# Kernel tuning notes

Measured on AMD Instinct MI355X. Metric: run time of the kernel, lower is better.

The kernel has to match this reference:

```python
import jax, jax.numpy as jnp
import numpy as np

B, T, F = 16, 1024, 512       # batch, time, input_dim
G, V, D = 2, 320, 128         # num_groups, num_vars, var_dim (quantized_dim // G)
TAU = 2.0                     # max_temp * decay**0 at num_updates=0
EPS = 1e-7


def setup_inputs() -> dict:
    key = jax.random.key(0)
    kx, kw, kc, kg = jax.random.split(key, 4)
    x = jax.random.normal(kx, (B, T, F), dtype=jnp.float32)
    w_proj = jax.random.normal(kw, (G * V, F), dtype=jnp.float32)  # NormalLinear: std=1
    b_proj = jnp.zeros((G * V,), dtype=jnp.float32)
    codebook = jax.random.uniform(kc, (1, G * V, D), dtype=jnp.float32)  # uniform init
    u = jax.random.uniform(kg, (B * T, G, V), dtype=jnp.float32, minval=1e-10, maxval=1.0)
    gumbel = -jnp.log(-jnp.log(u))
    return {"x": x, "w_proj": w_proj, "b_proj": b_proj, "codebook": codebook, "gumbel": gumbel}


def reference(x, w_proj, b_proj, codebook, gumbel):
    bsz, tsz, _ = x.shape
    # projection -> (B, T, G, V)
    logits = (jnp.einsum("btf,nf->btn", x, w_proj) + b_proj).reshape(bsz, tsz, G, V)

    # hard one-hot of argmax (float32), like scatter_
    k = jnp.argmax(logits, axis=-1)
    hard_x = jax.nn.one_hot(k, V, dtype=jnp.float32)  # (B, T, G, V)

    # code perplexity: mean over batch dim only, sum over (T, G)
    hard_probs = hard_x.mean(axis=0)  # (T, G, V)
    code_perplexity = jnp.exp(-jnp.sum(hard_probs * jnp.log(hard_probs + EPS), axis=-1)).sum()

    # prob perplexity: softmax over codes, mean over all tokens, sum over groups
    flat_logits = logits.reshape(bsz * tsz, G, V)
    avg_probs = jax.nn.softmax(flat_logits, axis=-1).mean(axis=0)  # (G, V)
    prob_perplexity = jnp.exp(-jnp.sum(avg_probs * jnp.log(avg_probs + EPS), axis=-1)).sum()

    # gumbel-softmax, hard=True with straight-through estimator (training path)
    y_soft = jax.nn.softmax((flat_logits + gumbel) / TAU, axis=-1)  # (N, G, V)
    idx = jnp.argmax(y_soft, axis=-1)
    y_hard = jax.nn.one_hot(idx, V, dtype=y_soft.dtype)
    y = y_hard + y_soft - jax.lax.stop_gradient(y_soft)  # (N, G, V)

    # broadcast-multiply + sum over codes == grouped gather/matmul against codebook
    cb_gvd = codebook.reshape(G, V, D)
    quantized = jnp.einsum("ngv,gvd->ngd", y, cb_gvd).reshape(bsz, tsz, G * D)
    return quantized, code_perplexity, prob_perplexity
```

## Files before the change

kernel.cpp:

```cpp
#include <hip/hip_runtime.h>
#include <math.h>

#define B_   16
#define T_   1024
#define F_   512
#define G_   2
#define V_   320
#define D_   128
#define N_   (B_ * T_)
#define GV   (G_ * V_)
#define EPS_ 1e-7f

#define ROWS    64
#define THREADS 512
#define NBLK    (N_ / ROWS)
#define NC      32

#define BOFF  0
#define AOFF  40960
#define BUFSZ 45056
#define LDSZ  (2 * BUFSZ)

typedef _Float16 half8 __attribute__((ext_vector_type(8)));
typedef _Float16 half2_t __attribute__((ext_vector_type(2)));
typedef float f32x16 __attribute__((ext_vector_type(16)));

#define GLDS16(g, l)                                                           \
  __builtin_amdgcn_global_load_lds(                                            \
      (const __attribute__((address_space(1))) unsigned int*)(g),              \
      (__attribute__((address_space(3))) unsigned int*)(l), 16, 0, 0)

#define CNTW      (T_ * G_ * (V_ / 2))
#define WS_COUNTS 0
#define WS_AVG    CNTW
#define WS_ENT    (WS_AVG + NBLK * GV)
#define WS_WPK    (WS_ENT + T_ * G_)
#define WS_AVGRED (WS_WPK + (GV * F_ * 2 / 2))

__global__ __launch_bounds__(640) void k_conv_w(
    const float* __restrict__ w, _Float16* __restrict__ wpk)
{
  const int cl = blockIdx.x;
  const int c = cl >> 1, limb = cl & 1;
#pragma unroll
  for (int it = 0; it < 2; ++it) {
    const int t2 = threadIdx.x + it * 640;
    const int n = t2 >> 6, ln = t2 & 63;
    const int row = n * 32 + (ln & 31);
    const int k0 = c * 16 + (ln >> 5) * 8;
    const float4 v0 = *(const float4*)(w + (size_t)row * F_ + k0);
    const float4 v1 = *(const float4*)(w + (size_t)row * F_ + k0 + 4);
    half8 h;
#pragma unroll
    for (int k = 0; k < 8; ++k) {
      const float vk = (k < 4) ? ((const float*)&v0)[k] : ((const float*)&v1)[k - 4];
      const _Float16 hk = (_Float16)vk;
      h[k] = limb ? (_Float16)((vk - (float)hk) * 2048.0f) : hk;
    }
    ((half8*)wpk)[((size_t)cl * 20 + n) * 64 + ln] = h;
  }
}

__global__ __launch_bounds__(THREADS, 2) void k_fused(
    const float* __restrict__ x, const _Float16* __restrict__ wpk,
    const float* __restrict__ bias, const float* __restrict__ cb,
    const float* __restrict__ gum, float* __restrict__ out,
    unsigned* __restrict__ counts, float* __restrict__ avg_part)
{
  __shared__ __align__(16) unsigned char SB[LDSZ];
  const int tid = threadIdx.x;
  const int wv  = tid >> 6;
  const int ln  = tid & 63;
  const int lo  = ln & 31, hi = ln >> 5;
  const int wvm = wv >> 2, wvn = wv & 3;
  const int blk = blockIdx.x;
  const int n0  = blk * ROWS;

  f32x16 ah_acc[5], al_acc[5];
#pragma unroll
  for (int t = 0; t < 5; ++t)
#pragma unroll
    for (int i = 0; i < 16; ++i) { ah_acc[t][i] = 0.0f; al_acc[t][i] = 0.0f; }

  const int arow = tid >> 3;
  const int akp  = tid & 7;
  const int awoff = (arow >> 5) * 1024 + (((akp >> 2) << 5) + (arow & 31)) * 16
                  + (akp & 3) * 4;
  const float2* x2 = (const float2*)x;
  const size_t xrowbase = (size_t)(n0 + arow) * (F_ / 2) + akp;

  const int aro_h = AOFF + 0 * 2048 + wvm * 1024 + ln * 16;
  const int aro_l = AOFF + 1 * 2048 + wvm * 1024 + ln * 16;
  int bro_h[5], bro_l[5];
#pragma unroll
  for (int t = 0; t < 5; ++t) {
    bro_h[t] = BOFF + (0 * 20 + wvn * 5 + t) * 1024 + ln * 16;
    bro_l[t] = BOFF + (1 * 20 + wvn * 5 + t) * 1024 + ln * 16;
  }

  {
    const float2 xv = x2[xrowbase + 0 * 8];
#pragma unroll
    for (int i = 0; i < 5; ++i) {
      const int seg = wv * 5 + i;
      GLDS16(wpk + ((size_t)(0 * 40 + seg) * 64 + ln) * 8, SB + BOFF + seg * 1024);
    }
    half2_t hh, hl;
#pragma unroll
    for (int k = 0; k < 2; ++k) {
      const float f = k ? xv.y : xv.x;
      const _Float16 h = (_Float16)f;
      hh[k] = h; hl[k] = (_Float16)((f - (float)h) * 2048.0f);
    }
    *(half2_t*)(SB + AOFF + awoff) = hh;
    *(half2_t*)(SB + AOFF + 2048 + awoff) = hl;
  }
  __builtin_amdgcn_sched_barrier(0);
  asm volatile("s_waitcnt vmcnt(0) lgkmcnt(0)" ::: "memory");
  __builtin_amdgcn_s_barrier();
  __builtin_amdgcn_sched_barrier(0);

  for (int cc = 0; cc < NC; ++cc) {
    unsigned char* curb = SB + (cc & 1) * BUFSZ;
    unsigned char* nxtb = SB + ((cc & 1) ^ 1) * BUFSZ;
    if (cc + 1 < NC) {
      const int c1 = cc + 1;
      const float2 xv = x2[xrowbase + c1 * 8];
#pragma unroll
      for (int i = 0; i < 5; ++i) {
        const int seg = wv * 5 + i;
        GLDS16(wpk + ((size_t)(c1 * 40 + seg) * 64 + ln) * 8,
               nxtb + BOFF + seg * 1024);
      }
      half2_t hh, hl;
#pragma unroll
      for (int k = 0; k < 2; ++k) {
        const float f = k ? xv.y : xv.x;
        const _Float16 h = (_Float16)f;
        hh[k] = h; hl[k] = (_Float16)((f - (float)h) * 2048.0f);
      }
      *(half2_t*)(nxtb + AOFF + awoff) = hh;
      *(half2_t*)(nxtb + AOFF + 2048 + awoff) = hl;
    }
    const half8 ah = *(const half8*)(curb + aro_h);
    const half8 al = *(const half8*)(curb + aro_l);
#pragma unroll
    for (int t = 0; t < 5; ++t) {
      const half8 bh = *(const half8*)(curb + bro_h[t]);
      const half8 bl = *(const half8*)(curb + bro_l[t]);
      ah_acc[t] = __builtin_amdgcn_mfma_f32_32x32x16_f16(ah, bh, ah_acc[t], 0, 0, 0);
      al_acc[t] = __builtin_amdgcn_mfma_f32_32x32x16_f16(al, bh, al_acc[t], 0, 0, 0);
      al_acc[t] = __builtin_amdgcn_mfma_f32_32x32x16_f16(ah, bl, al_acc[t], 0, 0, 0);
    }
    __builtin_amdgcn_sched_barrier(0);
    asm volatile("s_waitcnt vmcnt(0) lgkmcnt(0)" ::: "memory");
    __builtin_amdgcn_s_barrier();
    __builtin_amdgcn_sched_barrier(0);
  }

  float bfrag[5];
#pragma unroll
  for (int t = 0; t < 5; ++t) bfrag[t] = bias[wvn * 160 + t * 32 + lo];

  float racc[G_][5];
#pragma unroll
  for (int g = 0; g < G_; ++g)
#pragma unroll
    for (int j = 0; j < 5; ++j) racc[g][j] = 0.f;

  float* LBUF = (float*)SB;

#pragma unroll
  for (int R = 0; R < 4; ++R) {
    if (wvm == (R >> 1)) {
#pragma unroll
      for (int t = 0; t < 5; ++t) {
        const int col = wvn * 160 + t * 32 + lo;
#pragma unroll
        for (int rr = 0; rr < 8; ++rr) {
          const int reg  = ((R & 1) << 3) + rr;
          const int lrow = (rr & 3) + ((rr >> 2) << 3) + (hi << 2);
          LBUF[lrow * GV + col] =
              ah_acc[t][reg] + al_acc[t][reg] * (1.0f / 2048.0f) + bfrag[t];
        }
      }
    }
    __syncthreads();
#pragma unroll
    for (int rr2 = 0; rr2 < 2; ++rr2) {
      const int lrow = wv * 2 + rr2;
      const int n = n0 + R * 16 + lrow;
#pragma unroll
      for (int g = 0; g < G_; ++g) {
        float L[5], GU[5];
#pragma unroll
        for (int j = 0; j < 5; ++j) {
          L[j]  = LBUF[lrow * GV + g * V_ + 64 * j + ln];
          GU[j] = gum[(size_t)n * GV + g * V_ + 64 * j + ln];
        }
        float m1 = L[0];         int a1 = ln;
        float m2 = L[0] + GU[0]; int a2 = ln;
#pragma unroll
        for (int j = 1; j < 5; ++j) {
          const int cix = 64 * j + ln;
          if (L[j] > m1) { m1 = L[j]; a1 = cix; }
          const float t2 = L[j] + GU[j];
          if (t2 > m2) { m2 = t2; a2 = cix; }
        }
        for (int off = 32; off; off >>= 1) {
          float om = __shfl_down(m1, off); int oa = __shfl_down(a1, off);
          if (om > m1 || (om == m1 && oa < a1)) { m1 = om; a1 = oa; }
          float om2 = __shfl_down(m2, off); int oa2 = __shfl_down(a2, off);
          if (om2 > m2 || (om2 == m2 && oa2 < a2)) { m2 = om2; a2 = oa2; }
        }
        m1 = __shfl(m1, 0); a1 = __shfl(a1, 0); a2 = __shfl(a2, 0);

        float e[5], s = 0.f;
#pragma unroll
        for (int j = 0; j < 5; ++j) { e[j] = expf(L[j] - m1); s += e[j]; }
        for (int off = 32; off; off >>= 1) s += __shfl_down(s, off);
        s = __shfl(s, 0);
        const float inv = 1.0f / s;
#pragma unroll
        for (int j = 0; j < 5; ++j) racc[g][j] += e[j] * inv;

        if (ln == 0) {
          const int t = n & (T_ - 1);
          atomicAdd(&counts[(t * G_ + g) * (V_ / 2) + (a1 >> 1)],
                    1u << ((a1 & 1) * 16));
        }
        const float2* cbr = (const float2*)(cb + (size_t)(g * V_ + a2) * D_);
        float2* op = (float2*)(out + (size_t)n * (G_ * D_) + g * D_);
        op[ln] = cbr[ln];
      }
    }
    __syncthreads();
  }

  float* la = (float*)SB;
#pragma unroll
  for (int g = 0; g < G_; ++g)
#pragma unroll
    for (int j = 0; j < 5; ++j)
      la[wv * GV + g * V_ + 64 * j + ln] = racc[g][j];
  __syncthreads();
  for (int cix = tid; cix < GV; cix += THREADS) {
    float s = 0.f;
#pragma unroll
    for (int v = 0; v < 8; ++v) s += la[v * GV + cix];
    avg_part[(size_t)blk * GV + cix] = s;
  }
}

__global__ __launch_bounds__(256) void k_post(
    const unsigned* __restrict__ counts, float* __restrict__ ent,
    const float* __restrict__ avg_part, float* __restrict__ avgred)
{
  const int b = blockIdx.x;
  const int lane = threadIdx.x & 63;
  if (b < (T_ * G_) / 4) {
    const int item = b * 4 + (threadIdx.x >> 6);
    const unsigned* c = counts + (size_t)item * (V_ / 2);
    float s = 0.f;
#pragma unroll
    for (int j = 0; j < 3; ++j) {
      const int wi = lane + 64 * j;
      if (wi < V_ / 2) {
        const unsigned wd = c[wi];
        const float h0 = (float)(wd & 0xffffu) * (1.0f / B_);
        const float h1 = (float)(wd >> 16) * (1.0f / B_);
        s += h0 * logf(h0 + EPS_) + h1 * logf(h1 + EPS_);
      }
    }
    for (int off = 32; off; off >>= 1) s += __shfl_down(s, off);
    if (lane == 0) ent[item] = expf(-s);
  } else {
    const int cix = (b - (T_ * G_) / 4) * 4 + (threadIdx.x >> 6);
    float s = 0.f;
    for (int bb = lane; bb < NBLK; bb += 64) s += avg_part[(size_t)bb * GV + cix];
    for (int off = 32; off; off >>= 1) s += __shfl_down(s, off);
    if (lane == 0) avgred[cix] = s;
  }
}

__global__ __launch_bounds__(GV) void k_final(
    const float* __restrict__ avgred, const float* __restrict__ ent,
    float* __restrict__ out2)
{
  __shared__ float sh[GV];
  __shared__ float shc[GV];
  const int tid = threadIdx.x;

  const float p = avgred[tid] * (1.0f / N_);
  sh[tid] = p * logf(p + EPS_);

  float cs = 0.f;
  for (int i = tid; i < T_ * G_; i += GV) cs += ent[i];
  shc[tid] = cs;
  __syncthreads();

  if (tid < 64) {
    float s0 = 0.f, s1 = 0.f, sc = 0.f;
    for (int j = tid; j < V_; j += 64) { s0 += sh[j]; s1 += sh[V_ + j]; }
    for (int j = tid; j < GV; j += 64) sc += shc[j];
    for (int off = 32; off; off >>= 1) {
      s0 += __shfl_down(s0, off);
      s1 += __shfl_down(s1, off);
      sc += __shfl_down(sc, off);
    }
    if (tid == 0) {
      out2[0] = sc;
      out2[1] = expf(-s0) + expf(-s1);
    }
  }
}

extern "C" void kernel_launch(void* const* d_in, const int* in_sizes, int n_in,
                              void* d_out, int out_size, void* d_ws, size_t ws_size,
                              hipStream_t stream) {
  const float* x   = (const float*)d_in[0];
  const float* w   = (const float*)d_in[1];
  const float* b   = (const float*)d_in[2];
  const float* cb  = (const float*)d_in[3];
  const float* gum = (const float*)d_in[4];
  float* out = (float*)d_out;
  float* ws  = (float*)d_ws;

  unsigned* counts = (unsigned*)(ws + WS_COUNTS);
  float* avgp   = ws + WS_AVG;
  float* ent    = ws + WS_ENT;
  _Float16* wpk = (_Float16*)(ws + WS_WPK);
  float* avgred = ws + WS_AVGRED;

  hipMemsetAsync(counts, 0, (size_t)CNTW * sizeof(unsigned), stream);
  k_conv_w<<<64, 640, 0, stream>>>(w, wpk);
  k_fused<<<NBLK, THREADS, 0, stream>>>(x, wpk, b, cb, gum, out, counts, avgp);
  k_post<<<(T_ * G_) / 4 + GV / 4, 256, 0, stream>>>(counts, ent, avgp, avgred);
  k_final<<<1, GV, 0, stream>>>(avgred, ent, out + (size_t)N_ * G_ * D_);
}
```

Before: 188.6 us.

## Restructure fused GEMM to transposed register-resident tiles without LDS staging

The projection GEMM is reorganised so each wave computes W·xᵀ for one group and half of the codes across 32 rows. W fragments are loaded straight from global memory and x is converted to split-fp16 in registers, which removes the double-buffered LDS pipeline and its barriers. Bias is folded into the accumulator init. Argmax and softmax now run on registers, with one cross-wave exchange through LDS, and a transposed LDS pass produces the per-block probability sums. The memset of counts is folded into the weight-conversion kernel, saving a launch. In exchange, every wave re-reads W from global/L2 with no LDS reuse, and register pressure is high (Lv and e arrays).

```diff
diff --git a/kernel.cpp b/kernel.cpp
--- a/kernel.cpp
+++ b/kernel.cpp
@@ -16,19 +16,9 @@
 #define NBLK    (N_ / ROWS)
 #define NC      32
 
-#define BOFF  0
-#define AOFF  40960
-#define BUFSZ 45056
-#define LDSZ  (2 * BUFSZ)
-
 typedef _Float16 half8 __attribute__((ext_vector_type(8)));
-typedef _Float16 half2_t __attribute__((ext_vector_type(2)));
+typedef _Float16 half4 __attribute__((ext_vector_type(4)));
 typedef float f32x16 __attribute__((ext_vector_type(16)));
-
-#define GLDS16(g, l)                                                           \
-  __builtin_amdgcn_global_load_lds(                                            \
-      (const __attribute__((address_space(1))) unsigned int*)(g),              \
-      (__attribute__((address_space(3))) unsigned int*)(l), 16, 0, 0)
 
 #define CNTW      (T_ * G_ * (V_ / 2))
 #define WS_COUNTS 0
@@ -38,15 +28,19 @@
 #define WS_AVGRED (WS_WPK + (GV * F_ * 2 / 2))
 
 __global__ __launch_bounds__(640) void k_conv_w(
-    const float* __restrict__ w, _Float16* __restrict__ wpk)
+    const float* __restrict__ w, _Float16* __restrict__ wpk,
+    unsigned* __restrict__ counts)
 {
   const int cl = blockIdx.x;
   const int c = cl >> 1, limb = cl & 1;
 #pragma unroll
+  for (int z = 0; z < 8; ++z)
+    counts[(size_t)z * 40960 + blockIdx.x * 640 + threadIdx.x] = 0u;
+#pragma unroll
   for (int it = 0; it < 2; ++it) {
     const int t2 = threadIdx.x + it * 640;
-    const int n = t2 >> 6, ln = t2 & 63;
-    const int row = n * 32 + (ln & 31);
+    const int m = t2 >> 6, ln = t2 & 63;
+    const int row = m * 32 + (ln & 31);
     const int k0 = c * 16 + (ln >> 5) * 8;
     const float4 v0 = *(const float4*)(w + (size_t)row * F_ + k0);
     const float4 v1 = *(const float4*)(w + (size_t)row * F_ + k0 + 4);
@@ -57,7 +51,7 @@
       const _Float16 hk = (_Float16)vk;
       h[k] = limb ? (_Float16)((vk - (float)hk) * 2048.0f) : hk;
     }
-    ((half8*)wpk)[((size_t)cl * 20 + n) * 64 + ln] = h;
+    ((half8*)wpk)[((size_t)cl * 20 + m) * 64 + ln] = h;
   }
 }
 
@@ -67,188 +61,156 @@
     const float* __restrict__ gum, float* __restrict__ out,
     unsigned* __restrict__ counts, float* __restrict__ avg_part)
 {
-  __shared__ __align__(16) unsigned char SB[LDSZ];
+  __shared__ float PLDS[32][644];
+  __shared__ float XCH[8][32][4];
   const int tid = threadIdx.x;
   const int wv  = tid >> 6;
   const int ln  = tid & 63;
   const int lo  = ln & 31, hi = ln >> 5;
-  const int wvm = wv >> 2, wvn = wv & 3;
+  const int tq  = wv & 1;
+  const int g   = (wv >> 1) & 1;
+  const int mh  = wv >> 2;
   const int blk = blockIdx.x;
   const int n0  = blk * ROWS;
-
-  f32x16 ah_acc[5], al_acc[5];
+  const int n   = n0 + tq * 32 + lo;
+  const int codebase = g * 320 + mh * 160;
+
+  f32x16 ah[5], al[5];
+#pragma unroll
+  for (int t = 0; t < 5; ++t) {
+#pragma unroll
+    for (int q = 0; q < 4; ++q) {
+      const float4 b4 = *(const float4*)(bias + codebase + t * 32 + q * 8 + 4 * hi);
+#pragma unroll
+      for (int rr = 0; rr < 4; ++rr) {
+        ah[t][q * 4 + rr] = ((const float*)&b4)[rr];
+        al[t][q * 4 + rr] = 0.0f;
+      }
+    }
+  }
+
+  const half8* wp8 = (const half8*)wpk;
+  const float4* x4 = (const float4*)x;
+  const size_t xbase = (size_t)n * (F_ / 4) + hi * 2;
+
+  for (int c = 0; c < NC; ++c) {
+    const float4 v0 = x4[xbase + c * 4];
+    const float4 v1 = x4[xbase + c * 4 + 1];
+    half8 bh, bl;
+#pragma unroll
+    for (int k = 0; k < 8; ++k) {
+      const float f = (k < 4) ? ((const float*)&v0)[k] : ((const float*)&v1)[k - 4];
+      const _Float16 h = (_Float16)f;
+      bh[k] = h;
+      bl[k] = (_Float16)((f - (float)h) * 2048.0f);
+    }
+#pragma unroll
+    for (int t = 0; t < 5; ++t) {
+      const int m = g * 10 + mh * 5 + t;
+      const half8 wh8 = wp8[((size_t)(c * 2 + 0) * 20 + m) * 64 + ln];
+      const half8 wl8 = wp8[((size_t)(c * 2 + 1) * 20 + m) * 64 + ln];
+      ah[t] = __builtin_amdgcn_mfma_f32_32x32x16_f16(wh8, bh, ah[t], 0, 0, 0);
+      al[t] = __builtin_amdgcn_mfma_f32_32x32x16_f16(wl8, bh, al[t], 0, 0, 0);
+      al[t] = __builtin_amdgcn_mfma_f32_32x32x16_f16(wh8, bl, al[t], 0, 0, 0);
+    }
+  }
+
+  float Lv[5][16];
 #pragma unroll
   for (int t = 0; t < 5; ++t)
 #pragma unroll
-    for (int i = 0; i < 16; ++i) { ah_acc[t][i] = 0.0f; al_acc[t][i] = 0.0f; }
-
-  const int arow = tid >> 3;
-  const int akp  = tid & 7;
-  const int awoff = (arow >> 5) * 1024 + (((akp >> 2) << 5) + (arow & 31)) * 16
-                  + (akp & 3) * 4;
-  const float2* x2 = (const float2*)x;
-  const size_t xrowbase = (size_t)(n0 + arow) * (F_ / 2) + akp;
-
-  const int aro_h = AOFF + 0 * 2048 + wvm * 1024 + ln * 16;
-  const int aro_l = AOFF + 1 * 2048 + wvm * 1024 + ln * 16;
-  int bro_h[5], bro_l[5];
-#pragma unroll
-  for (int t = 0; t < 5; ++t) {
-    bro_h[t] = BOFF + (0 * 20 + wvn * 5 + t) * 1024 + ln * 16;
-    bro_l[t] = BOFF + (1 * 20 + wvn * 5 + t) * 1024 + ln * 16;
-  }
-
+    for (int i = 0; i < 16; ++i)
+      Lv[t][i] = ah[t][i] + al[t][i] * (1.0f / 2048.0f);
+
+  float m1 = -1e30f, m2 = -1e30f;
+  int a1 = 0, a2 = 0;
+#pragma unroll
+  for (int t = 0; t < 5; ++t)
+#pragma unroll
+    for (int q = 0; q < 4; ++q) {
+      const float4 gu = *(const float4*)(gum + (size_t)n * GV + codebase +
+                                         t * 32 + q * 8 + 4 * hi);
+#pragma unroll
+      for (int rr = 0; rr < 4; ++rr) {
+        const int cix = codebase + t * 32 + q * 8 + rr + 4 * hi;
+        const float v = Lv[t][q * 4 + rr];
+        if (v > m1 || (v == m1 && cix < a1)) { m1 = v; a1 = cix; }
+        const float v2 = v + ((const float*)&gu)[rr];
+        if (v2 > m2 || (v2 == m2 && cix < a2)) { m2 = v2; a2 = cix; }
+      }
+    }
   {
-    const float2 xv = x2[xrowbase + 0 * 8];
-#pragma unroll
-    for (int i = 0; i < 5; ++i) {
-      const int seg = wv * 5 + i;
-      GLDS16(wpk + ((size_t)(0 * 40 + seg) * 64 + ln) * 8, SB + BOFF + seg * 1024);
-    }
-    half2_t hh, hl;
-#pragma unroll
-    for (int k = 0; k < 2; ++k) {
-      const float f = k ? xv.y : xv.x;
-      const _Float16 h = (_Float16)f;
-      hh[k] = h; hl[k] = (_Float16)((f - (float)h) * 2048.0f);
-    }
-    *(half2_t*)(SB + AOFF + awoff) = hh;
-    *(half2_t*)(SB + AOFF + 2048 + awoff) = hl;
-  }
-  __builtin_amdgcn_sched_barrier(0);
-  asm volatile("s_waitcnt vmcnt(0) lgkmcnt(0)" ::: "memory");
-  __builtin_amdgcn_s_barrier();
-  __builtin_amdgcn_sched_barrier(0);
-
-  for (int cc = 0; cc < NC; ++cc) {
-    unsigned char* curb = SB + (cc & 1) * BUFSZ;
-    unsigned char* nxtb = SB + ((cc & 1) ^ 1) * BUFSZ;
-    if (cc + 1 < NC) {
-      const int c1 = cc + 1;
-      const float2 xv = x2[xrowbase + c1 * 8];
-#pragma unroll
-      for (int i = 0; i < 5; ++i) {
-        const int seg = wv * 5 + i;
-        GLDS16(wpk + ((size_t)(c1 * 40 + seg) * 64 + ln) * 8,
-               nxtb + BOFF + seg * 1024);
-      }
-      half2_t hh, hl;
-#pragma unroll
-      for (int k = 0; k < 2; ++k) {
-        const float f = k ? xv.y : xv.x;
-        const _Float16 h = (_Float16)f;
-        hh[k] = h; hl[k] = (_Float16)((f - (float)h) * 2048.0f);
-      }
-      *(half2_t*)(nxtb + AOFF + awoff) = hh;
-      *(half2_t*)(nxtb + AOFF + 2048 + awoff) = hl;
-    }
-    const half8 ah = *(const half8*)(curb + aro_h);
-    const half8 al = *(const half8*)(curb + aro_l);
-#pragma unroll
-    for (int t = 0; t < 5; ++t) {
-      const half8 bh = *(const half8*)(curb + bro_h[t]);
-      const half8 bl = *(const half8*)(curb + bro_l[t]);
-      ah_acc[t] = __builtin_amdgcn_mfma_f32_32x32x16_f16(ah, bh, ah_acc[t], 0, 0, 0);
-      al_acc[t] = __builtin_amdgcn_mfma_f32_32x32x16_f16(al, bh, al_acc[t], 0, 0, 0);
-      al_acc[t] = __builtin_amdgcn_mfma_f32_32x32x16_f16(ah, bl, al_acc[t], 0, 0, 0);
-    }
-    __builtin_amdgcn_sched_barrier(0);
-    asm volatile("s_waitcnt vmcnt(0) lgkmcnt(0)" ::: "memory");
-    __builtin_amdgcn_s_barrier();
-    __builtin_amdgcn_sched_barrier(0);
-  }
-
-  float bfrag[5];
-#pragma unroll
-  for (int t = 0; t < 5; ++t) bfrag[t] = bias[wvn * 160 + t * 32 + lo];
-
-  float racc[G_][5];
-#pragma unroll
-  for (int g = 0; g < G_; ++g)
-#pragma unroll
-    for (int j = 0; j < 5; ++j) racc[g][j] = 0.f;
-
-  float* LBUF = (float*)SB;
-
-#pragma unroll
-  for (int R = 0; R < 4; ++R) {
-    if (wvm == (R >> 1)) {
-#pragma unroll
-      for (int t = 0; t < 5; ++t) {
-        const int col = wvn * 160 + t * 32 + lo;
-#pragma unroll
-        for (int rr = 0; rr < 8; ++rr) {
-          const int reg  = ((R & 1) << 3) + rr;
-          const int lrow = (rr & 3) + ((rr >> 2) << 3) + (hi << 2);
-          LBUF[lrow * GV + col] =
-              ah_acc[t][reg] + al_acc[t][reg] * (1.0f / 2048.0f) + bfrag[t];
+    const float om = __shfl_xor(m1, 32); const int oa = __shfl_xor(a1, 32);
+    if (om > m1 || (om == m1 && oa < a1)) { m1 = om; a1 = oa; }
+    const float om2 = __shfl_xor(m2, 32); const int oa2 = __shfl_xor(a2, 32);
+    if (om2 > m2 || (om2 == m2 && oa2 < a2)) { m2 = om2; a2 = oa2; }
+  }
+  if (hi == 0) {
+    XCH[wv][lo][0] = m1;
+    XCH[wv][lo][1] = m2;
+    ((int*)&XCH[wv][lo][2])[0] = a1 | (a2 << 16);
+  }
+  __syncthreads();
+  const int pw = wv ^ 4;
+  {
+    const float pm1 = XCH[pw][lo][0], pm2 = XCH[pw][lo][1];
+    const int pa = ((const int*)&XCH[pw][lo][2])[0];
+    const int pa1 = pa & 0xffff, pa2 = (int)((unsigned)pa >> 16);
+    if (pm1 > m1 || (pm1 == m1 && pa1 < a1)) { m1 = pm1; a1 = pa1; }
+    if (pm2 > m2 || (pm2 == m2 && pa2 < a2)) { m2 = pm2; a2 = pa2; }
+  }
+  float e[5][16];
+  float s = 0.0f;
+#pragma unroll
+  for (int t = 0; t < 5; ++t)
+#pragma unroll
+    for (int i = 0; i < 16; ++i) { e[t][i] = expf(Lv[t][i] - m1); s += e[t][i]; }
+  s += __shfl_xor(s, 32);
+  if (hi == 0) XCH[wv][lo][3] = s;
+  __syncthreads();
+  const float inv = 1.0f / (s + XCH[pw][lo][3]);
+
+  float rsum0 = 0.0f, rsum1 = 0.0f;
+#pragma unroll
+  for (int r = 0; r < 2; ++r) {
+    if (r) __syncthreads();
+    if (tq == r) {
+#pragma unroll
+      for (int t = 0; t < 5; ++t)
+#pragma unroll
+        for (int q = 0; q < 4; ++q) {
+          float4 p4;
+#pragma unroll
+          for (int rr = 0; rr < 4; ++rr)
+            ((float*)&p4)[rr] = e[t][q * 4 + rr] * inv;
+          *(float4*)&PLDS[lo][codebase + t * 32 + q * 8 + 4 * hi] = p4;
         }
-      }
     }
     __syncthreads();
-#pragma unroll
-    for (int rr2 = 0; rr2 < 2; ++rr2) {
-      const int lrow = wv * 2 + rr2;
-      const int n = n0 + R * 16 + lrow;
-#pragma unroll
-      for (int g = 0; g < G_; ++g) {
-        float L[5], GU[5];
-#pragma unroll
-        for (int j = 0; j < 5; ++j) {
-          L[j]  = LBUF[lrow * GV + g * V_ + 64 * j + ln];
-          GU[j] = gum[(size_t)n * GV + g * V_ + 64 * j + ln];
-        }
-        float m1 = L[0];         int a1 = ln;
-        float m2 = L[0] + GU[0]; int a2 = ln;
-#pragma unroll
-        for (int j = 1; j < 5; ++j) {
-          const int cix = 64 * j + ln;
-          if (L[j] > m1) { m1 = L[j]; a1 = cix; }
-          const float t2 = L[j] + GU[j];
-          if (t2 > m2) { m2 = t2; a2 = cix; }
-        }
-        for (int off = 32; off; off >>= 1) {
-          float om = __shfl_down(m1, off); int oa = __shfl_down(a1, off);
-          if (om > m1 || (om == m1 && oa < a1)) { m1 = om; a1 = oa; }
-          float om2 = __shfl_down(m2, off); int oa2 = __shfl_down(a2, off);
-          if (om2 > m2 || (om2 == m2 && oa2 < a2)) { m2 = om2; a2 = oa2; }
-        }
-        m1 = __shfl(m1, 0); a1 = __shfl(a1, 0); a2 = __shfl(a2, 0);
-
-        float e[5], s = 0.f;
-#pragma unroll
-        for (int j = 0; j < 5; ++j) { e[j] = expf(L[j] - m1); s += e[j]; }
-        for (int off = 32; off; off >>= 1) s += __shfl_down(s, off);
-        s = __shfl(s, 0);
-        const float inv = 1.0f / s;
-#pragma unroll
-        for (int j = 0; j < 5; ++j) racc[g][j] += e[j] * inv;
-
-        if (ln == 0) {
-          const int t = n & (T_ - 1);
-          atomicAdd(&counts[(t * G_ + g) * (V_ / 2) + (a1 >> 1)],
-                    1u << ((a1 & 1) * 16));
-        }
-        const float2* cbr = (const float2*)(cb + (size_t)(g * V_ + a2) * D_);
-        float2* op = (float2*)(out + (size_t)n * (G_ * D_) + g * D_);
-        op[ln] = cbr[ln];
-      }
-    }
-    __syncthreads();
-  }
-
-  float* la = (float*)SB;
-#pragma unroll
-  for (int g = 0; g < G_; ++g)
-#pragma unroll
-    for (int j = 0; j < 5; ++j)
-      la[wv * GV + g * V_ + 64 * j + ln] = racc[g][j];
-  __syncthreads();
-  for (int cix = tid; cix < GV; cix += THREADS) {
-    float s = 0.f;
-#pragma unroll
-    for (int v = 0; v < 8; ++v) s += la[v * GV + cix];
-    avg_part[(size_t)blk * GV + cix] = s;
+    for (int i = 0; i < 32; ++i) {
+      const int tr = (ln + i) & 31;
+      rsum0 += PLDS[tr][tid];
+      if (tid < 128) rsum1 += PLDS[tr][512 + tid];
+    }
+  }
+  avg_part[(size_t)blk * GV + tid] = rsum0;
+  if (tid < 128) avg_part[(size_t)blk * GV + 512 + tid] = rsum1;
+
+  if (mh == 0) {
+    if (hi == 0) {
+      const int t_ = n & (T_ - 1);
+      const int va1 = a1 - g * V_;
+      atomicAdd(&counts[(t_ * G_ + g) * (V_ / 2) + (va1 >> 1)],
+                1u << ((va1 & 1) * 16));
+    }
+    const float2* cb2 = (const float2*)cb;
+    float2* o2 = (float2*)out;
+    for (int i = 0; i < 32; ++i) {
+      const int aa = __shfl(a2, i);
+      const int nn = n0 + tq * 32 + i;
+      o2[((size_t)nn * (G_ * D_) + g * D_) / 2 + ln] =
+          cb2[(size_t)aa * (D_ / 2) + ln];
+    }
   }
 }
 
@@ -332,8 +294,7 @@
   _Float16* wpk = (_Float16*)(ws + WS_WPK);
   float* avgred = ws + WS_AVGRED;
 
-  hipMemsetAsync(counts, 0, (size_t)CNTW * sizeof(unsigned), stream);
-  k_conv_w<<<64, 640, 0, stream>>>(w, wpk);
+  k_conv_w<<<64, 640, 0, stream>>>(w, wpk, counts);
   k_fused<<<NBLK, THREADS, 0, stream>>>(x, wpk, b, cb, gum, out, counts, avgp);
   k_post<<<(T_ * G_) / 4 + GV / 4, 256, 0, stream>>>(counts, ent, avgp, avgred);
   k_final<<<1, GV, 0, stream>>>(avgred, ent, out + (size_t)N_ * G_ * D_);
```

Result: no change. 187.5 us (-0.6%).

## Triple-buffer GEMM loads with prefetch depth two and fold counts zeroing into weight conversion

Applied to the files above, without the earlier changes.

Moves the projection GEMM main loop from double to triple buffering in LDS. Weight tiles are prefetched two chunks ahead and the x values one chunk ahead, and partial vmcnt waits let in-flight loads overlap the MFMAs. The count buffer is now zeroed inside the weight-conversion kernel, which drops the separate memset launch. The LDS footprint grows to about 132 KB, so launch bounds drop to one block per CU and occupancy is lower.

```diff
diff --git a/kernel.cpp b/kernel.cpp
--- a/kernel.cpp
+++ b/kernel.cpp
@@ -19,7 +19,7 @@
 #define BOFF  0
 #define AOFF  40960
 #define BUFSZ 45056
-#define LDSZ  (2 * BUFSZ)
+#define LDSZ  (3 * BUFSZ)
 
 typedef _Float16 half8 __attribute__((ext_vector_type(8)));
 typedef _Float16 half2_t __attribute__((ext_vector_type(2)));
@@ -38,15 +38,19 @@
 #define WS_AVGRED (WS_WPK + (GV * F_ * 2 / 2))
 
 __global__ __launch_bounds__(640) void k_conv_w(
-    const float* __restrict__ w, _Float16* __restrict__ wpk)
+    const float* __restrict__ w, _Float16* __restrict__ wpk,
+    unsigned* __restrict__ counts)
 {
   const int cl = blockIdx.x;
   const int c = cl >> 1, limb = cl & 1;
 #pragma unroll
+  for (int z = 0; z < 8; ++z)
+    counts[(size_t)z * 40960 + blockIdx.x * 640 + threadIdx.x] = 0u;
+#pragma unroll
   for (int it = 0; it < 2; ++it) {
     const int t2 = threadIdx.x + it * 640;
-    const int n = t2 >> 6, ln = t2 & 63;
-    const int row = n * 32 + (ln & 31);
+    const int m = t2 >> 6, ln = t2 & 63;
+    const int row = m * 32 + (ln & 31);
     const int k0 = c * 16 + (ln >> 5) * 8;
     const float4 v0 = *(const float4*)(w + (size_t)row * F_ + k0);
     const float4 v1 = *(const float4*)(w + (size_t)row * F_ + k0 + 4);
@@ -57,11 +61,11 @@
       const _Float16 hk = (_Float16)vk;
       h[k] = limb ? (_Float16)((vk - (float)hk) * 2048.0f) : hk;
     }
-    ((half8*)wpk)[((size_t)cl * 20 + n) * 64 + ln] = h;
-  }
-}
-
-__global__ __launch_bounds__(THREADS, 2) void k_fused(
+    ((half8*)wpk)[((size_t)cl * 20 + m) * 64 + ln] = h;
+  }
+}
+
+__global__ __launch_bounds__(THREADS, 1) void k_fused(
     const float* __restrict__ x, const _Float16* __restrict__ wpk,
     const float* __restrict__ bias, const float* __restrict__ cb,
     const float* __restrict__ gum, float* __restrict__ out,
@@ -98,13 +102,14 @@
     bro_l[t] = BOFF + (1 * 20 + wvn * 5 + t) * 1024 + ln * 16;
   }
 
-  {
-    const float2 xv = x2[xrowbase + 0 * 8];
+  auto STAGE_B = [&](int c, unsigned char* buf) {
 #pragma unroll
     for (int i = 0; i < 5; ++i) {
       const int seg = wv * 5 + i;
-      GLDS16(wpk + ((size_t)(0 * 40 + seg) * 64 + ln) * 8, SB + BOFF + seg * 1024);
-    }
+      GLDS16(wpk + ((size_t)(c * 40 + seg) * 64 + ln) * 8, buf + BOFF + seg * 1024);
+    }
+  };
+  auto STAGE_A = [&](float2 xv, unsigned char* buf) {
     half2_t hh, hl;
 #pragma unroll
     for (int k = 0; k < 2; ++k) {
@@ -112,48 +117,50 @@
       const _Float16 h = (_Float16)f;
       hh[k] = h; hl[k] = (_Float16)((f - (float)h) * 2048.0f);
     }
-    *(half2_t*)(SB + AOFF + awoff) = hh;
-    *(half2_t*)(SB + AOFF + 2048 + awoff) = hl;
-  }
+    *(half2_t*)(buf + AOFF + awoff) = hh;
+    *(half2_t*)(buf + AOFF + 2048 + awoff) = hl;
+  };
+
+  unsigned char* b0 = SB;
+  unsigned char* b1 = SB + BUFSZ;
+  unsigned char* b2 = SB + 2 * BUFSZ;
+
+  STAGE_B(0, b0);
+  const float2 xv0 = x2[xrowbase + 0 * 8];
+  STAGE_B(1, b1);
+  float2 xcur = x2[xrowbase + 1 * 8];
+  STAGE_A(xv0, b0);
   __builtin_amdgcn_sched_barrier(0);
-  asm volatile("s_waitcnt vmcnt(0) lgkmcnt(0)" ::: "memory");
+  asm volatile("s_waitcnt vmcnt(6) lgkmcnt(0)" ::: "memory");
   __builtin_amdgcn_s_barrier();
   __builtin_amdgcn_sched_barrier(0);
 
   for (int cc = 0; cc < NC; ++cc) {
-    unsigned char* curb = SB + (cc & 1) * BUFSZ;
-    unsigned char* nxtb = SB + ((cc & 1) ^ 1) * BUFSZ;
-    if (cc + 1 < NC) {
-      const int c1 = cc + 1;
-      const float2 xv = x2[xrowbase + c1 * 8];
-#pragma unroll
-      for (int i = 0; i < 5; ++i) {
-        const int seg = wv * 5 + i;
-        GLDS16(wpk + ((size_t)(c1 * 40 + seg) * 64 + ln) * 8,
-               nxtb + BOFF + seg * 1024);
+    float2 xnew = xcur;
+    if (cc + 2 < NC) {
+      STAGE_B(cc + 2, b2);
+      xnew = x2[xrowbase + (cc + 2) * 8];
+    }
+    if (cc + 1 < NC) STAGE_A(xcur, b1);
+    {
+      const half8 ahf = *(const half8*)(b0 + aro_h);
+      const half8 alf = *(const half8*)(b0 + aro_l);
+#pragma unroll
+      for (int t = 0; t < 5; ++t) {
+        const half8 bh = *(const half8*)(b0 + bro_h[t]);
+        const half8 bl = *(const half8*)(b0 + bro_l[t]);
+        ah_acc[t] = __builtin_amdgcn_mfma_f32_32x32x16_f16(ahf, bh, ah_acc[t], 0, 0, 0);
+        al_acc[t] = __builtin_amdgcn_mfma_f32_32x32x16_f16(alf, bh, al_acc[t], 0, 0, 0);
+        al_acc[t] = __builtin_amdgcn_mfma_f32_32x32x16_f16(ahf, bl, al_acc[t], 0, 0, 0);
       }
-      half2_t hh, hl;
-#pragma unroll
-      for (int k = 0; k < 2; ++k) {
-        const float f = k ? xv.y : xv.x;
-        const _Float16 h = (_Float16)f;
-        hh[k] = h; hl[k] = (_Float16)((f - (float)h) * 2048.0f);
-      }
-      *(half2_t*)(nxtb + AOFF + awoff) = hh;
-      *(half2_t*)(nxtb + AOFF + 2048 + awoff) = hl;
-    }
-    const half8 ah = *(const half8*)(curb + aro_h);
-    const half8 al = *(const half8*)(curb + aro_l);
-#pragma unroll
-    for (int t = 0; t < 5; ++t) {
-      const half8 bh = *(const half8*)(curb + bro_h[t]);
-      const half8 bl = *(const half8*)(curb + bro_l[t]);
-      ah_acc[t] = __builtin_amdgcn_mfma_f32_32x32x16_f16(ah, bh, ah_acc[t], 0, 0, 0);
-      al_acc[t] = __builtin_amdgcn_mfma_f32_32x32x16_f16(al, bh, al_acc[t], 0, 0, 0);
-      al_acc[t] = __builtin_amdgcn_mfma_f32_32x32x16_f16(ah, bl, al_acc[t], 0, 0, 0);
-    }
+    }
+    unsigned char* tmp = b0; b0 = b1; b1 = b2; b2 = tmp;
+    xcur = xnew;
     __builtin_amdgcn_sched_barrier(0);
-    asm volatile("s_waitcnt vmcnt(0) lgkmcnt(0)" ::: "memory");
+    if (cc + 2 < NC)
+      asm volatile("s_waitcnt vmcnt(6) lgkmcnt(0)" ::: "memory");
+    else
+      asm volatile("s_waitcnt vmcnt(0) lgkmcnt(0)" ::: "memory");
     __builtin_amdgcn_s_barrier();
     __builtin_amdgcn_sched_barrier(0);
   }
@@ -332,8 +339,7 @@
   _Float16* wpk = (_Float16*)(ws + WS_WPK);
   float* avgred = ws + WS_AVGRED;
 
-  hipMemsetAsync(counts, 0, (size_t)CNTW * sizeof(unsigned), stream);
-  k_conv_w<<<64, 640, 0, stream>>>(w, wpk);
+  k_conv_w<<<64, 640, 0, stream>>>(w, wpk, counts);
   k_fused<<<NBLK, THREADS, 0, stream>>>(x, wpk, b, cb, gum, out, counts, avgp);
   k_post<<<(T_ * G_) / 4 + GV / 4, 256, 0, stream>>>(counts, ent, avgp, avgred);
   k_final<<<1, GV, 0, stream>>>(avgred, ent, out + (size_t)N_ * G_ * D_);
```

Result: faster. 181.1 us (-4.0%).
